# Kernel tuning notes

Measured on AMD Instinct MI355X. Metric: run time of the kernel, lower is better.

The kernel has to match this reference:

```python
import jax, jax.numpy as jnp
import numpy as np

MEM_DIM = 1024
N_CHILD = 16384

def _linear_params(key, out_dim, in_dim):
    kw, kb = jax.random.split(key)
    bound = 1.0 / np.sqrt(in_dim)
    W = jax.random.uniform(kw, (out_dim, in_dim), jnp.float32, -bound, bound)
    b = jax.random.uniform(kb, (out_dim,), jnp.float32, -bound, bound)
    return W, b

def setup_inputs() -> dict:
    key = jax.random.key(0)
    ks = jax.random.split(key, 7)
    child_c = jax.random.normal(ks[0], (N_CHILD, MEM_DIM), jnp.float32)
    child_h = jax.random.normal(ks[1], (N_CHILD, MEM_DIM), jnp.float32)
    child_h_sum = jax.random.normal(ks[2], (MEM_DIM,), jnp.float32)
    W_ih, b_ih = _linear_params(ks[3], MEM_DIM, MEM_DIM)
    W_fh, b_fh = _linear_params(ks[4], MEM_DIM, MEM_DIM)
    W_uh, b_uh = _linear_params(ks[5], MEM_DIM, MEM_DIM)
    W_oh, b_oh = _linear_params(ks[6], MEM_DIM, MEM_DIM)
    return {
        "child_c": child_c, "child_h": child_h, "child_h_sum": child_h_sum,
        "W_ih": W_ih, "b_ih": b_ih, "W_fh": W_fh, "b_fh": b_fh,
        "W_uh": W_uh, "b_uh": b_uh, "W_oh": W_oh, "b_oh": b_oh,
    }

def reference(child_c, child_h, child_h_sum,
              W_ih, b_ih, W_fh, b_fh, W_uh, b_uh, W_oh, b_oh):
    # Gate projections on the summed child hidden state: [mem_dim]
    i = jax.nn.sigmoid(child_h_sum @ W_ih.T + b_ih)
    o = jax.nn.sigmoid(child_h_sum @ W_oh.T + b_oh)
    u = jnp.tanh(child_h_sum @ W_uh.T + b_uh)
    # Per-child forget gates, batched (replaces the Python loop): [N, mem_dim]
    f = jax.nn.sigmoid(child_h @ W_fh.T + b_fh)
    fc = f * child_c                     # [N, mem_dim]
    c = i * u + jnp.sum(fc, axis=0)      # [mem_dim]
    h = o * jnp.tanh(c)                  # [mem_dim]
    return (c, h)
```

## Files before the change

kernel.cpp:

```cpp
#include <hip/hip_runtime.h>
#include <hip/hip_bf16.h>
#include <math.h>

#define MEM_DIM 1024
#define N_CHILD 16384

#define BM 128
#define BN 128
#define BK 32
#define LDS_STRIDE 40

typedef __bf16 bf16_t;
typedef __bf16 bf16x4 __attribute__((ext_vector_type(4)));
typedef __bf16 bf16x8 __attribute__((ext_vector_type(8)));
typedef float f32x4 __attribute__((ext_vector_type(4)));

__global__ void gates_kernel(const float* __restrict__ hsum,
                             const float* __restrict__ W_ih, const float* __restrict__ b_ih,
                             const float* __restrict__ W_uh, const float* __restrict__ b_uh,
                             const float* __restrict__ W_oh, const float* __restrict__ b_oh,
                             float* __restrict__ acc_c, float* __restrict__ o_ws) {
    const int j = blockIdx.x;
    const int tid = threadIdx.x;
    const float* wi = W_ih + (size_t)j * MEM_DIM;
    const float* wu = W_uh + (size_t)j * MEM_DIM;
    const float* wo = W_oh + (size_t)j * MEM_DIM;
    float si = 0.f, su = 0.f, so = 0.f;
    for (int k = tid; k < MEM_DIM; k += 256) {
        float hv = hsum[k];
        si += wi[k] * hv;
        su += wu[k] * hv;
        so += wo[k] * hv;
    }
    for (int off = 32; off > 0; off >>= 1) {
        si += __shfl_down(si, off, 64);
        su += __shfl_down(su, off, 64);
        so += __shfl_down(so, off, 64);
    }
    __shared__ float red[3][4];
    const int wave = tid >> 6, lane = tid & 63;
    if (lane == 0) { red[0][wave] = si; red[1][wave] = su; red[2][wave] = so; }
    __syncthreads();
    if (tid == 0) {
        float ti = red[0][0] + red[0][1] + red[0][2] + red[0][3] + b_ih[j];
        float tu = red[1][0] + red[1][1] + red[1][2] + red[1][3] + b_uh[j];
        float to = red[2][0] + red[2][1] + red[2][2] + red[2][3] + b_oh[j];
        float iv = 1.f / (1.f + expf(-ti));
        float uv = tanhf(tu);
        float ov = 1.f / (1.f + expf(-to));
        acc_c[j] = iv * uv;
        o_ws[j]  = ov;
    }
}

__global__ __launch_bounds__(256) void fused_gemm(
        const float* __restrict__ child_h, const float* __restrict__ child_c,
        const float* __restrict__ W_fh, const float* __restrict__ b_fh,
        float* __restrict__ acc_c) {
    __shared__ __align__(16) bf16_t sA[BM * LDS_STRIDE];
    __shared__ __align__(16) bf16_t sB[BN * LDS_STRIDE];
    __shared__ float sred[BN];

    const int tid  = threadIdx.x;
    const int lane = tid & 63;
    const int wave = tid >> 6;
    const int wr = wave >> 1, wc = wave & 1;
    const int j0 = blockIdx.x * BN;
    const int n0 = blockIdx.y * BM;
    const int q = lane >> 4;
    const int cl = lane & 15;

    f32x4 acc[4][4];
#pragma unroll
    for (int a = 0; a < 4; a++)
#pragma unroll
        for (int b = 0; b < 4; b++) acc[a][b] = (f32x4)0.0f;

    for (int k0 = 0; k0 < MEM_DIM; k0 += BK) {
#pragma unroll
        for (int i = 0; i < 4; i++) {
            int f   = tid + i * 256;
            int row = f >> 3;
            int col = (f & 7) * 4;
            float4 va = *(const float4*)(child_h + (size_t)(n0 + row) * MEM_DIM + k0 + col);
            float4 vb = *(const float4*)(W_fh    + (size_t)(j0 + row) * MEM_DIM + k0 + col);
            bf16x4 ba = { (bf16_t)va.x, (bf16_t)va.y, (bf16_t)va.z, (bf16_t)va.w };
            bf16x4 bb = { (bf16_t)vb.x, (bf16_t)vb.y, (bf16_t)vb.z, (bf16_t)vb.w };
            *(bf16x4*)(&sA[row * LDS_STRIDE + col]) = ba;
            *(bf16x4*)(&sB[row * LDS_STRIDE + col]) = bb;
        }
        __syncthreads();

        bf16x8 afrag[4], bfrag[4];
#pragma unroll
        for (int mt = 0; mt < 4; mt++) {
            afrag[mt] = *(const bf16x8*)(&sA[(wr * 64 + mt * 16 + cl) * LDS_STRIDE + q * 8]);
            bfrag[mt] = *(const bf16x8*)(&sB[(wc * 64 + mt * 16 + cl) * LDS_STRIDE + q * 8]);
        }
#pragma unroll
        for (int mt = 0; mt < 4; mt++)
#pragma unroll
            for (int nt = 0; nt < 4; nt++)
                acc[mt][nt] = __builtin_amdgcn_mfma_f32_16x16x32_bf16(
                    afrag[mt], bfrag[nt], acc[mt][nt], 0, 0, 0);
        __syncthreads();
    }

    if (tid < BN) sred[tid] = 0.0f;
    __syncthreads();

    float colsum[4] = {0.f, 0.f, 0.f, 0.f};
#pragma unroll
    for (int nt = 0; nt < 4; nt++) {
        const int col = j0 + wc * 64 + nt * 16 + cl;
        const float bias = b_fh[col];
#pragma unroll
        for (int mt = 0; mt < 4; mt++) {
#pragma unroll
            for (int r = 0; r < 4; r++) {
                const int row = n0 + wr * 64 + mt * 16 + q * 4 + r;
                float s = acc[mt][nt][r] + bias;
                float fg = 1.0f / (1.0f + __expf(-s));
                colsum[nt] += fg * child_c[(size_t)row * MEM_DIM + col];
            }
        }
        colsum[nt] += __shfl_xor(colsum[nt], 16, 64);
        colsum[nt] += __shfl_xor(colsum[nt], 32, 64);
    }
    if (q == 0) {
#pragma unroll
        for (int nt = 0; nt < 4; nt++)
            atomicAdd(&sred[wc * 64 + nt * 16 + cl], colsum[nt]);
    }
    __syncthreads();
    if (tid < BN) atomicAdd(&acc_c[j0 + tid], sred[tid]);
}

__global__ void finalize_kernel(const float* __restrict__ acc_c,
                                const float* __restrict__ o_ws,
                                float* __restrict__ out) {
    int t = blockIdx.x * 256 + threadIdx.x;
    if (t < MEM_DIM) {
        float cv = acc_c[t];
        float hv = o_ws[t] * tanhf(cv);
        out[t] = cv;
        out[MEM_DIM + t] = hv;
    }
}

extern "C" void kernel_launch(void* const* d_in, const int* in_sizes, int n_in,
                              void* d_out, int out_size, void* d_ws, size_t ws_size,
                              hipStream_t stream) {
    const float* child_c = (const float*)d_in[0];
    const float* child_h = (const float*)d_in[1];
    const float* hsum    = (const float*)d_in[2];
    const float* W_ih    = (const float*)d_in[3];
    const float* b_ih    = (const float*)d_in[4];
    const float* W_fh    = (const float*)d_in[5];
    const float* b_fh    = (const float*)d_in[6];
    const float* W_uh    = (const float*)d_in[7];
    const float* b_uh    = (const float*)d_in[8];
    const float* W_oh    = (const float*)d_in[9];
    const float* b_oh    = (const float*)d_in[10];
    float* out   = (float*)d_out;
    float* acc_c = (float*)d_ws;
    float* o_ws  = acc_c + MEM_DIM;

    gates_kernel<<<MEM_DIM, 256, 0, stream>>>(hsum, W_ih, b_ih, W_uh, b_uh, W_oh, b_oh,
                                              acc_c, o_ws);
    dim3 grid(MEM_DIM / BN, N_CHILD / BM);
    fused_gemm<<<grid, 256, 0, stream>>>(child_h, child_c, W_fh, b_fh, acc_c);
    finalize_kernel<<<(MEM_DIM + 255) / 256, 256, 0, stream>>>(acc_c, o_ws, out);
}
```

Before: 255.0 us.

## Pre-convert inputs to bf16 and stream tiles into LDS via async global_load_lds

Adds conversion kernels that write child_h and W_fh to bf16 in workspace. A new GEMM then loads tiles straight from global memory into LDS with global_load_lds, using an XOR swizzle in place of a padded stride. The aim is to halve the bytes each GEMM tile reads repeatedly and to remove the per-element conversion and register round-trip from the main loop. In exchange it adds an extra full pass over the 64MB child_h (read fp32, write bf16), and the old path is kept as a fallback when the workspace is too small.

```diff
diff --git a/kernel.cpp b/kernel.cpp
--- a/kernel.cpp
+++ b/kernel.cpp
@@ -8,12 +8,33 @@
 #define BM 128
 #define BN 128
 #define BK 32
-#define LDS_STRIDE 40
+#define KITERS (MEM_DIM / BK)
 
 typedef __bf16 bf16_t;
 typedef __bf16 bf16x4 __attribute__((ext_vector_type(4)));
 typedef __bf16 bf16x8 __attribute__((ext_vector_type(8)));
 typedef float f32x4 __attribute__((ext_vector_type(4)));
+
+__device__ __forceinline__ int swz(int r) { return (r >> 1) & 3; }
+
+__device__ __forceinline__ void async_load16(const bf16_t* g, bf16_t* l) {
+    __builtin_amdgcn_global_load_lds(
+        (const __attribute__((address_space(1))) unsigned int*)g,
+        (__attribute__((address_space(3))) unsigned int*)l,
+        16, 0, 0);
+}
+
+__global__ __launch_bounds__(256) void cvt_bf16_kernel(const float* __restrict__ src,
+                                                       bf16_t* __restrict__ dst, int n8) {
+    int t = blockIdx.x * 256 + threadIdx.x;
+    if (t < n8) {
+        const float4* s = (const float4*)src + (size_t)t * 2;
+        float4 a = s[0], b = s[1];
+        bf16x8 o = { (bf16_t)a.x, (bf16_t)a.y, (bf16_t)a.z, (bf16_t)a.w,
+                     (bf16_t)b.x, (bf16_t)b.y, (bf16_t)b.z, (bf16_t)b.w };
+        *(bf16x8*)(dst + (size_t)t * 8) = o;
+    }
+}
 
 __global__ void gates_kernel(const float* __restrict__ hsum,
                              const float* __restrict__ W_ih, const float* __restrict__ b_ih,
@@ -53,35 +74,127 @@
     }
 }
 
-__global__ __launch_bounds__(256) void fused_gemm(
+__global__ __launch_bounds__(256) void fused_gemm_bf16(
+        const bf16_t* __restrict__ hbf, const bf16_t* __restrict__ wbf,
+        const float* __restrict__ child_c, const float* __restrict__ b_fh,
+        float* __restrict__ acc_c) {
+    __shared__ __align__(1024) bf16_t sA[BM * BK];
+    __shared__ __align__(1024) bf16_t sB[BN * BK];
+    __shared__ float sred[BN];
+
+    const int tid  = threadIdx.x;
+    const int lane = tid & 63;
+    const int wave = tid >> 6;
+    const int wr = wave >> 1, wc = wave & 1;
+    const int j0 = blockIdx.x * BN;
+    const int n0 = blockIdx.y * BM;
+    const int q  = lane >> 4;
+    const int cl = lane & 15;
+
+    const int seg = wave * 2;
+    const int r0 = seg * 16 + (lane >> 2);
+    const int r1 = r0 + 16;
+    const int p  = lane & 3;
+    const int c0 = p ^ swz(r0);
+    const int c1 = p ^ swz(r1);
+    const bf16_t* gA0 = hbf + (size_t)(n0 + r0) * MEM_DIM + c0 * 8;
+    const bf16_t* gA1 = hbf + (size_t)(n0 + r1) * MEM_DIM + c1 * 8;
+    const bf16_t* gB0 = wbf + (size_t)(j0 + r0) * MEM_DIM + c0 * 8;
+    const bf16_t* gB1 = wbf + (size_t)(j0 + r1) * MEM_DIM + c1 * 8;
+    bf16_t* lA0 = &sA[(seg)     * 512];
+    bf16_t* lA1 = &sA[(seg + 1) * 512];
+    bf16_t* lB0 = &sB[(seg)     * 512];
+    bf16_t* lB1 = &sB[(seg + 1) * 512];
+
+    int ofsA[4], ofsB[4];
+#pragma unroll
+    for (int mt = 0; mt < 4; mt++) {
+        int ra = wr * 64 + mt * 16 + cl;
+        int rb = wc * 64 + mt * 16 + cl;
+        ofsA[mt] = ra * BK + (q ^ swz(ra)) * 8;
+        ofsB[mt] = rb * BK + (q ^ swz(rb)) * 8;
+    }
+
+    f32x4 acc[4][4];
+#pragma unroll
+    for (int a = 0; a < 4; a++)
+#pragma unroll
+        for (int b = 0; b < 4; b++) acc[a][b] = (f32x4)0.0f;
+
+    for (int k = 0; k < KITERS; ++k) {
+        async_load16(gA0, lA0);
+        async_load16(gA1, lA1);
+        async_load16(gB0, lB0);
+        async_load16(gB1, lB1);
+        gA0 += BK; gA1 += BK; gB0 += BK; gB1 += BK;
+        __syncthreads();
+
+        bf16x8 af[4], bfr[4];
+#pragma unroll
+        for (int mt = 0; mt < 4; mt++) {
+            af[mt]  = *(const bf16x8*)(&sA[ofsA[mt]]);
+            bfr[mt] = *(const bf16x8*)(&sB[ofsB[mt]]);
+        }
+#pragma unroll
+        for (int mt = 0; mt < 4; mt++)
+#pragma unroll
+            for (int nt = 0; nt < 4; nt++)
+                acc[mt][nt] = __builtin_amdgcn_mfma_f32_16x16x32_bf16(
+                    af[mt], bfr[nt], acc[mt][nt], 0, 0, 0);
+        __syncthreads();
+    }
+
+    if (tid < BN) sred[tid] = 0.0f;
+    __syncthreads();
+
+    float colsum[4] = {0.f, 0.f, 0.f, 0.f};
+#pragma unroll
+    for (int nt = 0; nt < 4; nt++) {
+        const int col = j0 + wc * 64 + nt * 16 + cl;
+        const float bias = b_fh[col];
+#pragma unroll
+        for (int mt = 0; mt < 4; mt++) {
+#pragma unroll
+            for (int r = 0; r < 4; r++) {
+                const int row = n0 + wr * 64 + mt * 16 + q * 4 + r;
+                float s = acc[mt][nt][r] + bias;
+                float fg = 1.0f / (1.0f + __expf(-s));
+                colsum[nt] += fg * child_c[(size_t)row * MEM_DIM + col];
+            }
+        }
+        colsum[nt] += __shfl_xor(colsum[nt], 16, 64);
+        colsum[nt] += __shfl_xor(colsum[nt], 32, 64);
+    }
+    if (q == 0) {
+#pragma unroll
+        for (int nt = 0; nt < 4; nt++)
+            atomicAdd(&sred[wc * 64 + nt * 16 + cl], colsum[nt]);
+    }
+    __syncthreads();
+    if (tid < BN) atomicAdd(&acc_c[j0 + tid], sred[tid]);
+}
+
+#define LDS_STRIDE 40
+__global__ __launch_bounds__(256) void fused_gemm_f32(
         const float* __restrict__ child_h, const float* __restrict__ child_c,
         const float* __restrict__ W_fh, const float* __restrict__ b_fh,
         float* __restrict__ acc_c) {
     __shared__ __align__(16) bf16_t sA[BM * LDS_STRIDE];
     __shared__ __align__(16) bf16_t sB[BN * LDS_STRIDE];
     __shared__ float sred[BN];
-
-    const int tid  = threadIdx.x;
-    const int lane = tid & 63;
-    const int wave = tid >> 6;
+    const int tid = threadIdx.x, lane = tid & 63, wave = tid >> 6;
     const int wr = wave >> 1, wc = wave & 1;
-    const int j0 = blockIdx.x * BN;
-    const int n0 = blockIdx.y * BM;
-    const int q = lane >> 4;
-    const int cl = lane & 15;
-
+    const int j0 = blockIdx.x * BN, n0 = blockIdx.y * BM;
+    const int q = lane >> 4, cl = lane & 15;
     f32x4 acc[4][4];
 #pragma unroll
     for (int a = 0; a < 4; a++)
 #pragma unroll
         for (int b = 0; b < 4; b++) acc[a][b] = (f32x4)0.0f;
-
     for (int k0 = 0; k0 < MEM_DIM; k0 += BK) {
 #pragma unroll
         for (int i = 0; i < 4; i++) {
-            int f   = tid + i * 256;
-            int row = f >> 3;
-            int col = (f & 7) * 4;
+            int f = tid + i * 256, row = f >> 3, col = (f & 7) * 4;
             float4 va = *(const float4*)(child_h + (size_t)(n0 + row) * MEM_DIM + k0 + col);
             float4 vb = *(const float4*)(W_fh    + (size_t)(j0 + row) * MEM_DIM + k0 + col);
             bf16x4 ba = { (bf16_t)va.x, (bf16_t)va.y, (bf16_t)va.z, (bf16_t)va.w };
@@ -90,32 +203,28 @@
             *(bf16x4*)(&sB[row * LDS_STRIDE + col]) = bb;
         }
         __syncthreads();
-
-        bf16x8 afrag[4], bfrag[4];
+        bf16x8 af[4], bfr[4];
 #pragma unroll
         for (int mt = 0; mt < 4; mt++) {
-            afrag[mt] = *(const bf16x8*)(&sA[(wr * 64 + mt * 16 + cl) * LDS_STRIDE + q * 8]);
-            bfrag[mt] = *(const bf16x8*)(&sB[(wc * 64 + mt * 16 + cl) * LDS_STRIDE + q * 8]);
+            af[mt]  = *(const bf16x8*)(&sA[(wr * 64 + mt * 16 + cl) * LDS_STRIDE + q * 8]);
+            bfr[mt] = *(const bf16x8*)(&sB[(wc * 64 + mt * 16 + cl) * LDS_STRIDE + q * 8]);
         }
 #pragma unroll
         for (int mt = 0; mt < 4; mt++)
 #pragma unroll
             for (int nt = 0; nt < 4; nt++)
-                acc[mt][nt] = __builtin_amdgcn_mfma_f32_16x16x32_bf16(
-                    afrag[mt], bfrag[nt], acc[mt][nt], 0, 0, 0);
-        __syncthreads();
-    }
-
+                acc[mt][nt] = __builtin_amdgcn_mfma_f32_16x16x32_bf16(af[mt], bfr[nt], acc[mt][nt], 0, 0, 0);
+        __syncthreads();
+    }
     if (tid < BN) sred[tid] = 0.0f;
     __syncthreads();
-
     float colsum[4] = {0.f, 0.f, 0.f, 0.f};
 #pragma unroll
     for (int nt = 0; nt < 4; nt++) {
         const int col = j0 + wc * 64 + nt * 16 + cl;
         const float bias = b_fh[col];
 #pragma unroll
-        for (int mt = 0; mt < 4; mt++) {
+        for (int mt = 0; mt < 4; mt++)
 #pragma unroll
             for (int r = 0; r < 4; r++) {
                 const int row = n0 + wr * 64 + mt * 16 + q * 4 + r;
@@ -123,15 +232,13 @@
                 float fg = 1.0f / (1.0f + __expf(-s));
                 colsum[nt] += fg * child_c[(size_t)row * MEM_DIM + col];
             }
-        }
         colsum[nt] += __shfl_xor(colsum[nt], 16, 64);
         colsum[nt] += __shfl_xor(colsum[nt], 32, 64);
     }
-    if (q == 0) {
+    if (q == 0)
 #pragma unroll
         for (int nt = 0; nt < 4; nt++)
             atomicAdd(&sred[wc * 64 + nt * 16 + cl], colsum[nt]);
-    }
     __syncthreads();
     if (tid < BN) atomicAdd(&acc_c[j0 + tid], sred[tid]);
 }
@@ -163,12 +270,28 @@
     const float* W_oh    = (const float*)d_in[9];
     const float* b_oh    = (const float*)d_in[10];
     float* out   = (float*)d_out;
+
     float* acc_c = (float*)d_ws;
     float* o_ws  = acc_c + MEM_DIM;
+    const size_t HBF_OFF = 8192;
+    const size_t HBF_BYTES = (size_t)N_CHILD * MEM_DIM * 2;
+    const size_t WBF_BYTES = (size_t)MEM_DIM * MEM_DIM * 2;
+    const size_t NEED = HBF_OFF + HBF_BYTES + WBF_BYTES;
 
     gates_kernel<<<MEM_DIM, 256, 0, stream>>>(hsum, W_ih, b_ih, W_uh, b_uh, W_oh, b_oh,
                                               acc_c, o_ws);
     dim3 grid(MEM_DIM / BN, N_CHILD / BM);
-    fused_gemm<<<grid, 256, 0, stream>>>(child_h, child_c, W_fh, b_fh, acc_c);
+
+    if (ws_size >= NEED) {
+        bf16_t* hbf = (bf16_t*)((char*)d_ws + HBF_OFF);
+        bf16_t* wbf = (bf16_t*)((char*)d_ws + HBF_OFF + HBF_BYTES);
+        int n8_h = (N_CHILD * MEM_DIM) / 8;
+        int n8_w = (MEM_DIM * MEM_DIM) / 8;
+        cvt_bf16_kernel<<<(n8_h + 255) / 256, 256, 0, stream>>>(child_h, hbf, n8_h);
+        cvt_bf16_kernel<<<(n8_w + 255) / 256, 256, 0, stream>>>(W_fh, wbf, n8_w);
+        fused_gemm_bf16<<<grid, 256, 0, stream>>>(hbf, wbf, child_c, b_fh, acc_c);
+    } else {
+        fused_gemm_f32<<<grid, 256, 0, stream>>>(child_h, child_c, W_fh, b_fh, acc_c);
+    }
     finalize_kernel<<<(MEM_DIM + 255) / 256, 256, 0, stream>>>(acc_c, o_ws, out);
 }
```

Measured after the change: 227.2 us. -10.9%, faster.
